# Optimization experiments

Measured on AMD Instinct MI355X. Metric: run time of the kernel, lower is better.

Reference implementation:

```python
import jax, jax.numpy as jnp
import numpy as np

K = 2            # number of attention heads (k in __init__)
NEG = -9.0e15    # mask fill value from the torch code
N, C, CO = 6144, 128, 128


def _ln(x, g, b, eps=1e-5):
    m = x.mean(-1, keepdims=True)
    v = ((x - m) ** 2).mean(-1, keepdims=True)
    return (x - m) / jnp.sqrt(v + eps) * g + b


def setup_inputs() -> dict:
    key = jax.random.key(0)
    ks = jax.random.split(key, 6)
    x = jax.random.normal(ks[0], (N, C), jnp.float32)
    adj = (jax.random.uniform(ks[1], (N, N)) < 0.01).astype(jnp.float32)
    ff0_w = jax.random.normal(ks[2], (K, C, C), jnp.float32) / np.float32(np.sqrt(C))
    ff1_w = jax.random.normal(ks[3], (K, CO, C), jnp.float32) / np.float32(np.sqrt(C))
    attn_w = jax.random.normal(ks[4], (K, 2 * C), jnp.float32) / np.float32(np.sqrt(2 * C))
    return dict(
        x=x, adj=adj, ff0_w=ff0_w, ff1_w=ff1_w, attn_w=attn_w,
        g1=jnp.ones((C,), jnp.float32), b1=jnp.zeros((C,), jnp.float32),
        g2=jnp.ones((C,), jnp.float32), b2=jnp.zeros((C,), jnp.float32),
    )


def reference(x, adj, ff0_w, ff1_w, attn_w, g1, b1, g2, b2):
    n, c = x.shape
    co = ff1_w.shape[1]
    x_norm = _ln(x, g1, b1)
    # torch does adj = adj + eye(n) each iteration; since adj >= 0 the mask
    # (adj > 0) is identical for every iteration: original edges plus self-loops.
    mask = (adj > 0) | jnp.eye(n, dtype=bool)
    h_next = jnp.zeros((n, co), x.dtype)
    for i in range(K):  # small fixed head count, structurally distinct weights
        h = x_norm @ ff0_w[i].T  # [n, c]
        # attn_fc(cat(h_i, h_j)) == a1.h_i + a2.h_j  (exact decomposition of
        # the concat+linear; avoids materializing the [n, n, 2c] tensor)
        s_src = h @ attn_w[i, :c]  # [n], contribution of row node i
        s_dst = h @ attn_w[i, c:]  # [n], contribution of col node j
        e = jax.nn.leaky_relu(s_src[:, None] + s_dst[None, :])  # [n, n]
        e = jnp.where(mask, e, jnp.float32(NEG))
        atten = jax.nn.softmax(e, axis=1)  # dropout p=0.0 -> identity
        att = atten @ h + x  # residual adds pre-norm x
        att = _ln(att, g2, b2)
        h_next = h_next + jax.nn.elu(att @ ff1_w[i].T) / K
    return h_next
```

## Files before the change

### kernel.cpp

```cpp
#include <hip/hip_runtime.h>
#include <math.h>

#define Nn 6144
#define Cc 128
#define NHD 2
#define GMAXDEG 256
#define FF0_BLOCKS 384

__global__ __launch_bounds__(256) void k_front(
    const float* __restrict__ x, const float* __restrict__ g1,
    const float* __restrict__ b1, const float* __restrict__ Bw,
    const float* __restrict__ aw, const float* __restrict__ adj,
    float* __restrict__ h, float* __restrict__ ssrc,
    float* __restrict__ sdst, int* __restrict__ degp,
    int* __restrict__ nbrg) {
  __shared__ __align__(16) float smem[128 * 36 + 64 * 132];
  const int t = threadIdx.x;
  const int bid = blockIdx.x;

  if (bid >= FF0_BLOCKS) {
    int* nbr = (int*)smem;
    __shared__ int cnt;
    const int r = bid - FF0_BLOCKS;
    if (t == 0) cnt = 0;
    __syncthreads();
    const float4* arow = (const float4*)(adj + (size_t)r * Nn);
    for (int i = t; i < Nn / 4; i += 256) {
      float4 v = arow[i];
      int j = i * 4;
      if (v.x > 0.f || j + 0 == r) { int p = atomicAdd(&cnt, 1); if (p < GMAXDEG) nbr[p] = j + 0; }
      if (v.y > 0.f || j + 1 == r) { int p = atomicAdd(&cnt, 1); if (p < GMAXDEG) nbr[p] = j + 1; }
      if (v.z > 0.f || j + 2 == r) { int p = atomicAdd(&cnt, 1); if (p < GMAXDEG) nbr[p] = j + 2; }
      if (v.w > 0.f || j + 3 == r) { int p = atomicAdd(&cnt, 1); if (p < GMAXDEG) nbr[p] = j + 3; }
    }
    __syncthreads();
    const int d = min(cnt, GMAXDEG);
    if (t == 0) degp[r] = d;
    for (int k = t; k < d; k += 256) nbrg[(size_t)r * GMAXDEG + k] = nbr[k];
    return;
  }

  float (*Axn)[36] = (float(*)[36])smem;
  float (*Bs)[132] = (float(*)[132])(smem + 128 * 36);
  const int head = bid & 1;
  const int row0 = (bid >> 1) * 32;
  const float* Bh = Bw + (size_t)head * Cc * Cc;

  {
    const int row = t >> 3, seg = t & 7;
    const int cb = seg * 16;
    const float* xr = x + (size_t)(row0 + row) * Cc + cb;
    float v[16], gg[16], bb[16];
#pragma unroll
    for (int i = 0; i < 16; i += 4) {
      float4 t4 = *(const float4*)(xr + i);
      v[i] = t4.x; v[i + 1] = t4.y; v[i + 2] = t4.z; v[i + 3] = t4.w;
      float4 g4 = *(const float4*)(g1 + cb + i);
      gg[i] = g4.x; gg[i + 1] = g4.y; gg[i + 2] = g4.z; gg[i + 3] = g4.w;
      float4 b4 = *(const float4*)(b1 + cb + i);
      bb[i] = b4.x; bb[i + 1] = b4.y; bb[i + 2] = b4.z; bb[i + 3] = b4.w;
    }
    float s = 0.f;
#pragma unroll
    for (int i = 0; i < 16; i++) s += v[i];
    s += __shfl_xor(s, 1); s += __shfl_xor(s, 2); s += __shfl_xor(s, 4);
    float mean = s * (1.0f / 128.0f);
    float q = 0.f;
#pragma unroll
    for (int i = 0; i < 16; i++) { float d_ = v[i] - mean; q += d_ * d_; }
    q += __shfl_xor(q, 1); q += __shfl_xor(q, 2); q += __shfl_xor(q, 4);
    float rstd = rsqrtf(q * (1.0f / 128.0f) + 1e-5f);
#pragma unroll
    for (int i = 0; i < 16; i++)
      Axn[cb + i][row] = (v[i] - mean) * rstd * gg[i] + bb[i];
  }
  __syncthreads();

  const int tr = t & 7, tc = t >> 3;
  float acc[4][4];
#pragma unroll
  for (int i = 0; i < 4; i++)
#pragma unroll
    for (int j = 0; j < 4; j++) acc[i][j] = 0.f;

  for (int kt = 0; kt < Cc; kt += 64) {
    for (int i = t; i < 2048; i += 256) {
      int cc2 = i >> 4, k4 = i & 15;
      float4 v = *(const float4*)(Bh + (size_t)cc2 * Cc + kt + k4 * 4);
      Bs[k4 * 4 + 0][cc2] = v.x; Bs[k4 * 4 + 1][cc2] = v.y;
      Bs[k4 * 4 + 2][cc2] = v.z; Bs[k4 * 4 + 3][cc2] = v.w;
    }
    __syncthreads();
#pragma unroll
    for (int k = 0; k < 64; k++) {
      float4 a4 = *(const float4*)&Axn[kt + k][tr * 4];
      float4 b4 = *(const float4*)&Bs[k][tc * 4];
      float av[4] = {a4.x, a4.y, a4.z, a4.w};
      float bv[4] = {b4.x, b4.y, b4.z, b4.w};
#pragma unroll
      for (int i = 0; i < 4; i++)
#pragma unroll
        for (int j = 0; j < 4; j++) acc[i][j] = fmaf(av[i], bv[j], acc[i][j]);
    }
    __syncthreads();
  }

  float psrc[4], pdst[4];
  {
    float4 w1 = *(const float4*)(aw + head * 2 * Cc + tc * 4);
    float4 w2 = *(const float4*)(aw + head * 2 * Cc + Cc + tc * 4);
#pragma unroll
    for (int i = 0; i < 4; i++) {
      float* op = h + ((size_t)head * Nn + row0 + tr * 4 + i) * Cc + tc * 4;
      *(float4*)op = make_float4(acc[i][0], acc[i][1], acc[i][2], acc[i][3]);
      psrc[i] = acc[i][0] * w1.x + acc[i][1] * w1.y + acc[i][2] * w1.z + acc[i][3] * w1.w;
      pdst[i] = acc[i][0] * w2.x + acc[i][1] * w2.y + acc[i][2] * w2.z + acc[i][3] * w2.w;
    }
  }
  float* epart = &Bs[0][0];
#pragma unroll
  for (int i = 0; i < 4; i++) {
    epart[((tc * 32) + (tr * 4 + i)) * 2 + 0] = psrc[i];
    epart[((tc * 32) + (tr * 4 + i)) * 2 + 1] = pdst[i];
  }
  __syncthreads();
  if (t < 64) {
    int row = t >> 1, s = t & 1;
    float v = 0.f;
#pragma unroll
    for (int g = 0; g < 32; g++) v += epart[(g * 32 + row) * 2 + s];
    (s ? sdst : ssrc)[head * Nn + row0 + row] = v;
  }
}

__global__ __launch_bounds__(256) void k_attn_wave(
    const int* __restrict__ degp, const int* __restrict__ nbrg,
    const float* __restrict__ x, const float* __restrict__ h,
    const float* __restrict__ ssrc, const float* __restrict__ sdst,
    const float* __restrict__ g2, const float* __restrict__ b2,
    float* __restrict__ att_out) {
  const int t = threadIdx.x;
  const int lane = t & 63;
  const int r = blockIdx.x * 4 + (t >> 6);
  const int deg = min(degp[r], 128);
  int nbr0 = r, nbr1 = r;
  if (lane < deg) nbr0 = nbrg[(size_t)r * GMAXDEG + lane];
  if (64 + lane < deg) nbr1 = nbrg[(size_t)r * GMAXDEG + 64 + lane];
  const float s0 = ssrc[r], s1 = ssrc[Nn + r];
  float e0a = -3.0e38f, e0b = -3.0e38f, e1a = -3.0e38f, e1b = -3.0e38f;
  if (lane < deg) {
    float v0 = s0 + sdst[nbr0], v1 = s1 + sdst[Nn + nbr0];
    e0a = (v0 > 0.f) ? v0 : 0.01f * v0;
    e1a = (v1 > 0.f) ? v1 : 0.01f * v1;
  }
  if (64 + lane < deg) {
    float v0 = s0 + sdst[nbr1], v1 = s1 + sdst[Nn + nbr1];
    e0b = (v0 > 0.f) ? v0 : 0.01f * v0;
    e1b = (v1 > 0.f) ? v1 : 0.01f * v1;
  }
  float m0 = fmaxf(e0a, e0b), m1 = fmaxf(e1a, e1b);
#pragma unroll
  for (int o = 32; o; o >>= 1) {
    m0 = fmaxf(m0, __shfl_xor(m0, o));
    m1 = fmaxf(m1, __shfl_xor(m1, o));
  }
  float w0a = __expf(e0a - m0), w0b = __expf(e0b - m0);
  float w1a = __expf(e1a - m1), w1b = __expf(e1b - m1);
  float l0 = w0a + w0b, l1 = w1a + w1b;
#pragma unroll
  for (int o = 32; o; o >>= 1) { l0 += __shfl_xor(l0, o); l1 += __shfl_xor(l1, o); }
  const float inv0 = 1.0f / l0, inv1 = 1.0f / l1;
  const int c2 = lane * 2;
  const float* h0p = h + c2;
  const float* h1p = h + (size_t)Nn * Cc + c2;
  float a0x = 0.f, a0y = 0.f, a1x = 0.f, a1y = 0.f;
  for (int k = 0; k < deg; ++k) {
    const bool lo = (k < 64);
    const int ksel = k & 63;
    int j = __shfl(lo ? nbr0 : nbr1, ksel);
    float w0 = __shfl(lo ? w0a : w0b, ksel);
    float w1 = __shfl(lo ? w1a : w1b, ksel);
    float2 hv0 = *(const float2*)(h0p + (size_t)j * Cc);
    float2 hv1 = *(const float2*)(h1p + (size_t)j * Cc);
    a0x = fmaf(w0, hv0.x, a0x); a0y = fmaf(w0, hv0.y, a0y);
    a1x = fmaf(w1, hv1.x, a1x); a1y = fmaf(w1, hv1.y, a1y);
  }
  float2 xv = *(const float2*)(x + (size_t)r * Cc + c2);
  a0x = fmaf(a0x, inv0, xv.x); a0y = fmaf(a0y, inv0, xv.y);
  a1x = fmaf(a1x, inv1, xv.x); a1y = fmaf(a1y, inv1, xv.y);
  float t0 = a0x + a0y, t1 = a1x + a1y;
#pragma unroll
  for (int o = 32; o; o >>= 1) { t0 += __shfl_xor(t0, o); t1 += __shfl_xor(t1, o); }
  float mu0 = t0 * (1.0f / 128.0f), mu1 = t1 * (1.0f / 128.0f);
  float d0x = a0x - mu0, d0y = a0y - mu0;
  float d1x = a1x - mu1, d1y = a1y - mu1;
  float q0 = d0x * d0x + d0y * d0y, q1 = d1x * d1x + d1y * d1y;
#pragma unroll
  for (int o = 32; o; o >>= 1) { q0 += __shfl_xor(q0, o); q1 += __shfl_xor(q1, o); }
  float rs0 = rsqrtf(q0 * (1.0f / 128.0f) + 1e-5f);
  float rs1 = rsqrtf(q1 * (1.0f / 128.0f) + 1e-5f);
  float2 gv = *(const float2*)(g2 + c2);
  float2 bv = *(const float2*)(b2 + c2);
  *(float2*)(att_out + ((size_t)r) * Cc + c2) =
      make_float2(d0x * rs0 * gv.x + bv.x, d0y * rs0 * gv.y + bv.y);
  *(float2*)(att_out + ((size_t)Nn + r) * Cc + c2) =
      make_float2(d1x * rs1 * gv.x + bv.x, d1y * rs1 * gv.y + bv.y);
}

__global__ __launch_bounds__(256) void k_ff1_comb(const float* __restrict__ A,
                                                  const float* __restrict__ Bw,
                                                  float* __restrict__ out) {
  __shared__ float As[64][36];
  __shared__ float Bs[64][132];
  const int t = threadIdx.x;
  const int row0 = blockIdx.x * 32;
  const int tr = t & 7, tc = t >> 3;
  float sum[4][4];
#pragma unroll
  for (int i = 0; i < 4; i++)
#pragma unroll
    for (int j = 0; j < 4; j++) sum[i][j] = 0.f;

  for (int head = 0; head < NHD; head++) {
    const float* Ah = A + (size_t)head * Nn * Cc;
    const float* Bh = Bw + (size_t)head * Cc * Cc;
    float acc[4][4];
#pragma unroll
    for (int i = 0; i < 4; i++)
#pragma unroll
      for (int j = 0; j < 4; j++) acc[i][j] = 0.f;

    for (int kt = 0; kt < Cc; kt += 64) {
      __syncthreads();
      for (int i = t; i < 512; i += 256) {
        int rr = i >> 4, k4 = i & 15;
        float4 v = *(const float4*)(Ah + (size_t)(row0 + rr) * Cc + kt + k4 * 4);
        As[k4 * 4 + 0][rr] = v.x; As[k4 * 4 + 1][rr] = v.y;
        As[k4 * 4 + 2][rr] = v.z; As[k4 * 4 + 3][rr] = v.w;
      }
      for (int i = t; i < 2048; i += 256) {
        int cc2 = i >> 4, k4 = i & 15;
        float4 v = *(const float4*)(Bh + (size_t)cc2 * Cc + kt + k4 * 4);
        Bs[k4 * 4 + 0][cc2] = v.x; Bs[k4 * 4 + 1][cc2] = v.y;
        Bs[k4 * 4 + 2][cc2] = v.z; Bs[k4 * 4 + 3][cc2] = v.w;
      }
      __syncthreads();
#pragma unroll
      for (int k = 0; k < 64; k++) {
        float4 a4 = *(const float4*)&As[k][tr * 4];
        float4 b4 = *(const float4*)&Bs[k][tc * 4];
        float av[4] = {a4.x, a4.y, a4.z, a4.w};
        float bv[4] = {b4.x, b4.y, b4.z, b4.w};
#pragma unroll
        for (int i = 0; i < 4; i++)
#pragma unroll
          for (int j = 0; j < 4; j++) acc[i][j] = fmaf(av[i], bv[j], acc[i][j]);
      }
    }
#pragma unroll
    for (int i = 0; i < 4; i++)
#pragma unroll
      for (int j = 0; j < 4; j++) {
        float v = acc[i][j];
        v = (v > 0.f) ? v : (expf(v) - 1.f);
        sum[i][j] = fmaf(v, 0.5f, sum[i][j]);
      }
  }
#pragma unroll
  for (int i = 0; i < 4; i++) {
    float* op = out + (size_t)(row0 + tr * 4 + i) * Cc + tc * 4;
    *(float4*)op = make_float4(sum[i][0], sum[i][1], sum[i][2], sum[i][3]);
  }
}

extern "C" void kernel_launch(void* const* d_in, const int* in_sizes, int n_in,
                              void* d_out, int out_size, void* d_ws, size_t ws_size,
                              hipStream_t stream) {
  const float* x   = (const float*)d_in[0];
  const float* adj = (const float*)d_in[1];
  const float* ff0 = (const float*)d_in[2];
  const float* ff1 = (const float*)d_in[3];
  const float* aw  = (const float*)d_in[4];
  const float* g1  = (const float*)d_in[5];
  const float* b1  = (const float*)d_in[6];
  const float* g2  = (const float*)d_in[7];
  const float* b2  = (const float*)d_in[8];
  float* out = (float*)d_out;

  float* ws   = (float*)d_ws;
  float* h    = ws;
  float* ssrc = h + (size_t)2 * Nn * Cc;
  float* sdst = ssrc + 2 * Nn;
  float* attn = sdst + 2 * Nn;
  int* degp   = (int*)(attn + (size_t)2 * Nn * Cc);
  int* nbrg   = degp + Nn;

  hipLaunchKernelGGL(k_front, dim3(FF0_BLOCKS + Nn), dim3(256), 0, stream,
                     x, g1, b1, ff0, aw, adj, h, ssrc, sdst, degp, nbrg);
  hipLaunchKernelGGL(k_attn_wave, dim3(Nn / 4), dim3(256), 0, stream,
                     degp, nbrg, x, h, ssrc, sdst, g2, b2, attn);
  hipLaunchKernelGGL(k_ff1_comb, dim3(Nn / 32), dim3(256), 0, stream, attn, ff1, out);
}
```

Baseline: 303.0 us.

## Fuse adjacency scan into attention kernel with wave ballot compaction

Moves the per-row adjacency scan out of the front kernel into the attention kernel, where each wave compacts its row's neighbours into LDS using ballot and popcount prefix sums instead of shared atomics. This removes the global neighbour-list write and read round trip and the atomic contention. In exchange, the large adjacency read no longer overlaps with the ff0 GEMM and runs inside the attention kernel with fewer waves per row.

```diff
diff --git a/kernel.cpp b/kernel.cpp
--- a/kernel.cpp
+++ b/kernel.cpp
@@ -4,46 +4,18 @@
 #define Nn 6144
 #define Cc 128
 #define NHD 2
-#define GMAXDEG 256
-#define FF0_BLOCKS 384
-
-__global__ __launch_bounds__(256) void k_front(
+#define WMAXDEG 128
+
+__global__ __launch_bounds__(256) void k_ff0_fused(
     const float* __restrict__ x, const float* __restrict__ g1,
     const float* __restrict__ b1, const float* __restrict__ Bw,
-    const float* __restrict__ aw, const float* __restrict__ adj,
-    float* __restrict__ h, float* __restrict__ ssrc,
-    float* __restrict__ sdst, int* __restrict__ degp,
-    int* __restrict__ nbrg) {
-  __shared__ __align__(16) float smem[128 * 36 + 64 * 132];
+    const float* __restrict__ aw, float* __restrict__ h,
+    float* __restrict__ ssrc, float* __restrict__ sdst) {
+  __shared__ float Axn[128][36];
+  __shared__ float Bs[64][132];
   const int t = threadIdx.x;
-  const int bid = blockIdx.x;
-
-  if (bid >= FF0_BLOCKS) {
-    int* nbr = (int*)smem;
-    __shared__ int cnt;
-    const int r = bid - FF0_BLOCKS;
-    if (t == 0) cnt = 0;
-    __syncthreads();
-    const float4* arow = (const float4*)(adj + (size_t)r * Nn);
-    for (int i = t; i < Nn / 4; i += 256) {
-      float4 v = arow[i];
-      int j = i * 4;
-      if (v.x > 0.f || j + 0 == r) { int p = atomicAdd(&cnt, 1); if (p < GMAXDEG) nbr[p] = j + 0; }
-      if (v.y > 0.f || j + 1 == r) { int p = atomicAdd(&cnt, 1); if (p < GMAXDEG) nbr[p] = j + 1; }
-      if (v.z > 0.f || j + 2 == r) { int p = atomicAdd(&cnt, 1); if (p < GMAXDEG) nbr[p] = j + 2; }
-      if (v.w > 0.f || j + 3 == r) { int p = atomicAdd(&cnt, 1); if (p < GMAXDEG) nbr[p] = j + 3; }
-    }
-    __syncthreads();
-    const int d = min(cnt, GMAXDEG);
-    if (t == 0) degp[r] = d;
-    for (int k = t; k < d; k += 256) nbrg[(size_t)r * GMAXDEG + k] = nbr[k];
-    return;
-  }
-
-  float (*Axn)[36] = (float(*)[36])smem;
-  float (*Bs)[132] = (float(*)[132])(smem + 128 * 36);
-  const int head = bid & 1;
-  const int row0 = (bid >> 1) * 32;
+  const int head = blockIdx.y;
+  const int row0 = blockIdx.x * 32;
   const float* Bh = Bw + (size_t)head * Cc * Cc;
 
   {
@@ -133,19 +105,53 @@
   }
 }
 
-__global__ __launch_bounds__(256) void k_attn_wave(
-    const int* __restrict__ degp, const int* __restrict__ nbrg,
-    const float* __restrict__ x, const float* __restrict__ h,
-    const float* __restrict__ ssrc, const float* __restrict__ sdst,
-    const float* __restrict__ g2, const float* __restrict__ b2,
-    float* __restrict__ att_out) {
+__global__ __launch_bounds__(256) void k_attn_hybrid(
+    const float* __restrict__ adj, const float* __restrict__ x,
+    const float* __restrict__ h, const float* __restrict__ ssrc,
+    const float* __restrict__ sdst, const float* __restrict__ g2,
+    const float* __restrict__ b2, float* __restrict__ att_out) {
+  __shared__ int nbrs[4][WMAXDEG];
   const int t = threadIdx.x;
   const int lane = t & 63;
-  const int r = blockIdx.x * 4 + (t >> 6);
-  const int deg = min(degp[r], 128);
+  const int wid = t >> 6;
+  const int r = blockIdx.x * 4 + wid;
+  int* nbrw = nbrs[wid];
+  int cnt = 0;
+  const float4* arow = (const float4*)(adj + (size_t)r * Nn);
+  const unsigned long long lmask = (lane == 63) ? 0x7fffffffffffffffull
+                                                : ((1ull << lane) - 1ull);
+  for (int i = lane; i < Nn / 4; i += 64) {
+    float4 v = arow[i];
+    int j = i * 4;
+    {
+      bool p = (v.x > 0.f) || (j == r);
+      unsigned long long m = __ballot(p);
+      if (p) { int pos = cnt + (int)__popcll(m & lmask); if (pos < WMAXDEG) nbrw[pos] = j; }
+      cnt += (int)__popcll(m);
+    }
+    {
+      bool p = (v.y > 0.f) || (j + 1 == r);
+      unsigned long long m = __ballot(p);
+      if (p) { int pos = cnt + (int)__popcll(m & lmask); if (pos < WMAXDEG) nbrw[pos] = j + 1; }
+      cnt += (int)__popcll(m);
+    }
+    {
+      bool p = (v.z > 0.f) || (j + 2 == r);
+      unsigned long long m = __ballot(p);
+      if (p) { int pos = cnt + (int)__popcll(m & lmask); if (pos < WMAXDEG) nbrw[pos] = j + 2; }
+      cnt += (int)__popcll(m);
+    }
+    {
+      bool p = (v.w > 0.f) || (j + 3 == r);
+      unsigned long long m = __ballot(p);
+      if (p) { int pos = cnt + (int)__popcll(m & lmask); if (pos < WMAXDEG) nbrw[pos] = j + 3; }
+      cnt += (int)__popcll(m);
+    }
+  }
+  const int deg = min(cnt, WMAXDEG);
   int nbr0 = r, nbr1 = r;
-  if (lane < deg) nbr0 = nbrg[(size_t)r * GMAXDEG + lane];
-  if (64 + lane < deg) nbr1 = nbrg[(size_t)r * GMAXDEG + 64 + lane];
+  if (lane < deg) nbr0 = nbrw[lane];
+  if (64 + lane < deg) nbr1 = nbrw[64 + lane];
   const float s0 = ssrc[r], s1 = ssrc[Nn + r];
   float e0a = -3.0e38f, e0b = -3.0e38f, e1a = -3.0e38f, e1b = -3.0e38f;
   if (lane < deg) {
@@ -292,12 +298,10 @@
   float* ssrc = h + (size_t)2 * Nn * Cc;
   float* sdst = ssrc + 2 * Nn;
   float* attn = sdst + 2 * Nn;
-  int* degp   = (int*)(attn + (size_t)2 * Nn * Cc);
-  int* nbrg   = degp + Nn;
-
-  hipLaunchKernelGGL(k_front, dim3(FF0_BLOCKS + Nn), dim3(256), 0, stream,
-                     x, g1, b1, ff0, aw, adj, h, ssrc, sdst, degp, nbrg);
-  hipLaunchKernelGGL(k_attn_wave, dim3(Nn / 4), dim3(256), 0, stream,
-                     degp, nbrg, x, h, ssrc, sdst, g2, b2, attn);
+
+  hipLaunchKernelGGL(k_ff0_fused, dim3(Nn / 32, NHD), dim3(256), 0, stream,
+                     x, g1, b1, ff0, aw, h, ssrc, sdst);
+  hipLaunchKernelGGL(k_attn_hybrid, dim3(Nn / 4), dim3(256), 0, stream,
+                     adj, x, h, ssrc, sdst, g2, b2, attn);
   hipLaunchKernelGGL(k_ff1_comb, dim3(Nn / 32), dim3(256), 0, stream, attn, ff1, out);
 }
```

Result: no change. 303.5 us (+0.2%).

## Split adjacency scan from ff0 GEMM and shrink GEMM tiles for more blocks

Applied to the files above, without the earlier changes.

Splits the combined front kernel into a separate adjacency-scan kernel and an ff0+layernorm+score kernel. The ff0 GEMM tile goes from 32 to 16 rows with a 2D grid over heads. The ff1 GEMM tile goes to 16 rows by 64 columns, which raises the block count to give more parallelism. The cost is an extra launch, the loss of overlap between the scan and the GEMM, and more redundant loads of the weight matrices across the smaller tiles.

```diff
diff --git a/kernel.cpp b/kernel.cpp
--- a/kernel.cpp
+++ b/kernel.cpp
@@ -5,54 +5,50 @@
 #define Cc 128
 #define NHD 2
 #define GMAXDEG 256
-#define FF0_BLOCKS 384
-
-__global__ __launch_bounds__(256) void k_front(
+
+__global__ __launch_bounds__(256) void k_scan(const float* __restrict__ adj,
+                                              int* __restrict__ degp,
+                                              int* __restrict__ nbrg) {
+  __shared__ int nbr[GMAXDEG];
+  __shared__ int cnt;
+  const int t = threadIdx.x;
+  const int r = blockIdx.x;
+  if (t == 0) cnt = 0;
+  __syncthreads();
+  const float4* arow = (const float4*)(adj + (size_t)r * Nn);
+  for (int i = t; i < Nn / 4; i += 256) {
+    float4 v = arow[i];
+    int j = i * 4;
+    if (v.x > 0.f || j + 0 == r) { int p = atomicAdd(&cnt, 1); if (p < GMAXDEG) nbr[p] = j + 0; }
+    if (v.y > 0.f || j + 1 == r) { int p = atomicAdd(&cnt, 1); if (p < GMAXDEG) nbr[p] = j + 1; }
+    if (v.z > 0.f || j + 2 == r) { int p = atomicAdd(&cnt, 1); if (p < GMAXDEG) nbr[p] = j + 2; }
+    if (v.w > 0.f || j + 3 == r) { int p = atomicAdd(&cnt, 1); if (p < GMAXDEG) nbr[p] = j + 3; }
+  }
+  __syncthreads();
+  const int d = min(cnt, GMAXDEG);
+  if (t == 0) degp[r] = d;
+  for (int k = t; k < d; k += 256) nbrg[(size_t)r * GMAXDEG + k] = nbr[k];
+}
+
+__global__ __launch_bounds__(256) void k_ff0_fused(
     const float* __restrict__ x, const float* __restrict__ g1,
     const float* __restrict__ b1, const float* __restrict__ Bw,
-    const float* __restrict__ aw, const float* __restrict__ adj,
-    float* __restrict__ h, float* __restrict__ ssrc,
-    float* __restrict__ sdst, int* __restrict__ degp,
-    int* __restrict__ nbrg) {
-  __shared__ __align__(16) float smem[128 * 36 + 64 * 132];
-  const int t = threadIdx.x;
-  const int bid = blockIdx.x;
-
-  if (bid >= FF0_BLOCKS) {
-    int* nbr = (int*)smem;
-    __shared__ int cnt;
-    const int r = bid - FF0_BLOCKS;
-    if (t == 0) cnt = 0;
-    __syncthreads();
-    const float4* arow = (const float4*)(adj + (size_t)r * Nn);
-    for (int i = t; i < Nn / 4; i += 256) {
-      float4 v = arow[i];
-      int j = i * 4;
-      if (v.x > 0.f || j + 0 == r) { int p = atomicAdd(&cnt, 1); if (p < GMAXDEG) nbr[p] = j + 0; }
-      if (v.y > 0.f || j + 1 == r) { int p = atomicAdd(&cnt, 1); if (p < GMAXDEG) nbr[p] = j + 1; }
-      if (v.z > 0.f || j + 2 == r) { int p = atomicAdd(&cnt, 1); if (p < GMAXDEG) nbr[p] = j + 2; }
-      if (v.w > 0.f || j + 3 == r) { int p = atomicAdd(&cnt, 1); if (p < GMAXDEG) nbr[p] = j + 3; }
-    }
-    __syncthreads();
-    const int d = min(cnt, GMAXDEG);
-    if (t == 0) degp[r] = d;
-    for (int k = t; k < d; k += 256) nbrg[(size_t)r * GMAXDEG + k] = nbr[k];
-    return;
-  }
-
-  float (*Axn)[36] = (float(*)[36])smem;
-  float (*Bs)[132] = (float(*)[132])(smem + 128 * 36);
-  const int head = bid & 1;
-  const int row0 = (bid >> 1) * 32;
+    const float* __restrict__ aw, float* __restrict__ h,
+    float* __restrict__ ssrc, float* __restrict__ sdst) {
+  __shared__ float Axn[128][18];
+  __shared__ float Bs[64][132];
+  const int t = threadIdx.x;
+  const int head = blockIdx.y;
+  const int row0 = blockIdx.x * 16;
   const float* Bh = Bw + (size_t)head * Cc * Cc;
 
   {
-    const int row = t >> 3, seg = t & 7;
-    const int cb = seg * 16;
+    const int row = t >> 4, seg = t & 15;
+    const int cb = seg * 8;
     const float* xr = x + (size_t)(row0 + row) * Cc + cb;
-    float v[16], gg[16], bb[16];
-#pragma unroll
-    for (int i = 0; i < 16; i += 4) {
+    float v[8], gg[8], bb[8];
+#pragma unroll
+    for (int i = 0; i < 8; i += 4) {
       float4 t4 = *(const float4*)(xr + i);
       v[i] = t4.x; v[i + 1] = t4.y; v[i + 2] = t4.z; v[i + 3] = t4.w;
       float4 g4 = *(const float4*)(g1 + cb + i);
@@ -62,24 +58,26 @@
     }
     float s = 0.f;
 #pragma unroll
-    for (int i = 0; i < 16; i++) s += v[i];
-    s += __shfl_xor(s, 1); s += __shfl_xor(s, 2); s += __shfl_xor(s, 4);
+    for (int i = 0; i < 8; i++) s += v[i];
+    s += __shfl_xor(s, 1); s += __shfl_xor(s, 2);
+    s += __shfl_xor(s, 4); s += __shfl_xor(s, 8);
     float mean = s * (1.0f / 128.0f);
     float q = 0.f;
 #pragma unroll
-    for (int i = 0; i < 16; i++) { float d_ = v[i] - mean; q += d_ * d_; }
-    q += __shfl_xor(q, 1); q += __shfl_xor(q, 2); q += __shfl_xor(q, 4);
+    for (int i = 0; i < 8; i++) { float d_ = v[i] - mean; q += d_ * d_; }
+    q += __shfl_xor(q, 1); q += __shfl_xor(q, 2);
+    q += __shfl_xor(q, 4); q += __shfl_xor(q, 8);
     float rstd = rsqrtf(q * (1.0f / 128.0f) + 1e-5f);
 #pragma unroll
-    for (int i = 0; i < 16; i++)
+    for (int i = 0; i < 8; i++)
       Axn[cb + i][row] = (v[i] - mean) * rstd * gg[i] + bb[i];
   }
   __syncthreads();
 
   const int tr = t & 7, tc = t >> 3;
-  float acc[4][4];
-#pragma unroll
-  for (int i = 0; i < 4; i++)
+  float acc[2][4];
+#pragma unroll
+  for (int i = 0; i < 2; i++)
 #pragma unroll
     for (int j = 0; j < 4; j++) acc[i][j] = 0.f;
 
@@ -93,25 +91,27 @@
     __syncthreads();
 #pragma unroll
     for (int k = 0; k < 64; k++) {
-      float4 a4 = *(const float4*)&Axn[kt + k][tr * 4];
+      float2 a2 = *(const float2*)&Axn[kt + k][tr * 2];
       float4 b4 = *(const float4*)&Bs[k][tc * 4];
-      float av[4] = {a4.x, a4.y, a4.z, a4.w};
-      float bv[4] = {b4.x, b4.y, b4.z, b4.w};
-#pragma unroll
-      for (int i = 0; i < 4; i++)
-#pragma unroll
-        for (int j = 0; j < 4; j++) acc[i][j] = fmaf(av[i], bv[j], acc[i][j]);
+      acc[0][0] = fmaf(a2.x, b4.x, acc[0][0]);
+      acc[0][1] = fmaf(a2.x, b4.y, acc[0][1]);
+      acc[0][2] = fmaf(a2.x, b4.z, acc[0][2]);
+      acc[0][3] = fmaf(a2.x, b4.w, acc[0][3]);
+      acc[1][0] = fmaf(a2.y, b4.x, acc[1][0]);
+      acc[1][1] = fmaf(a2.y, b4.y, acc[1][1]);
+      acc[1][2] = fmaf(a2.y, b4.z, acc[1][2]);
+      acc[1][3] = fmaf(a2.y, b4.w, acc[1][3]);
     }
     __syncthreads();
   }
 
-  float psrc[4], pdst[4];
+  float psrc[2], pdst[2];
   {
     float4 w1 = *(const float4*)(aw + head * 2 * Cc + tc * 4);
     float4 w2 = *(const float4*)(aw + head * 2 * Cc + Cc + tc * 4);
 #pragma unroll
-    for (int i = 0; i < 4; i++) {
-      float* op = h + ((size_t)head * Nn + row0 + tr * 4 + i) * Cc + tc * 4;
+    for (int i = 0; i < 2; i++) {
+      float* op = h + ((size_t)head * Nn + row0 + tr * 2 + i) * Cc + tc * 4;
       *(float4*)op = make_float4(acc[i][0], acc[i][1], acc[i][2], acc[i][3]);
       psrc[i] = acc[i][0] * w1.x + acc[i][1] * w1.y + acc[i][2] * w1.z + acc[i][3] * w1.w;
       pdst[i] = acc[i][0] * w2.x + acc[i][1] * w2.y + acc[i][2] * w2.z + acc[i][3] * w2.w;
@@ -119,16 +119,16 @@
   }
   float* epart = &Bs[0][0];
 #pragma unroll
-  for (int i = 0; i < 4; i++) {
-    epart[((tc * 32) + (tr * 4 + i)) * 2 + 0] = psrc[i];
-    epart[((tc * 32) + (tr * 4 + i)) * 2 + 1] = pdst[i];
-  }
-  __syncthreads();
-  if (t < 64) {
+  for (int i = 0; i < 2; i++) {
+    epart[(tc * 16 + tr * 2 + i) * 2 + 0] = psrc[i];
+    epart[(tc * 16 + tr * 2 + i) * 2 + 1] = pdst[i];
+  }
+  __syncthreads();
+  if (t < 32) {
     int row = t >> 1, s = t & 1;
     float v = 0.f;
 #pragma unroll
-    for (int g = 0; g < 32; g++) v += epart[(g * 32 + row) * 2 + s];
+    for (int g = 0; g < 32; g++) v += epart[(g * 16 + row) * 2 + s];
     (s ? sdst : ssrc)[head * Nn + row0 + row] = v;
   }
 }
@@ -210,66 +210,59 @@
 __global__ __launch_bounds__(256) void k_ff1_comb(const float* __restrict__ A,
                                                   const float* __restrict__ Bw,
                                                   float* __restrict__ out) {
-  __shared__ float As[64][36];
-  __shared__ float Bs[64][132];
-  const int t = threadIdx.x;
-  const int row0 = blockIdx.x * 32;
+  __shared__ float As[128][18];
+  __shared__ float Bs[64][68];
+  const int t = threadIdx.x;
+  const int row0 = blockIdx.x * 16;
+  const int c0 = blockIdx.y * 64;
   const int tr = t & 7, tc = t >> 3;
-  float sum[4][4];
-#pragma unroll
-  for (int i = 0; i < 4; i++)
-#pragma unroll
-    for (int j = 0; j < 4; j++) sum[i][j] = 0.f;
+  float sum[2][2];
+  sum[0][0] = sum[0][1] = sum[1][0] = sum[1][1] = 0.f;
 
   for (int head = 0; head < NHD; head++) {
     const float* Ah = A + (size_t)head * Nn * Cc;
     const float* Bh = Bw + (size_t)head * Cc * Cc;
-    float acc[4][4];
-#pragma unroll
-    for (int i = 0; i < 4; i++)
-#pragma unroll
-      for (int j = 0; j < 4; j++) acc[i][j] = 0.f;
-
+    __syncthreads();
+    for (int i = t; i < 512; i += 256) {
+      int rr = i >> 5, k4 = i & 31;
+      float4 v = *(const float4*)(Ah + (size_t)(row0 + rr) * Cc + k4 * 4);
+      As[k4 * 4 + 0][rr] = v.x; As[k4 * 4 + 1][rr] = v.y;
+      As[k4 * 4 + 2][rr] = v.z; As[k4 * 4 + 3][rr] = v.w;
+    }
+    float acc[2][2];
+    acc[0][0] = acc[0][1] = acc[1][0] = acc[1][1] = 0.f;
     for (int kt = 0; kt < Cc; kt += 64) {
-      __syncthreads();
-      for (int i = t; i < 512; i += 256) {
-        int rr = i >> 4, k4 = i & 15;
-        float4 v = *(const float4*)(Ah + (size_t)(row0 + rr) * Cc + kt + k4 * 4);
-        As[k4 * 4 + 0][rr] = v.x; As[k4 * 4 + 1][rr] = v.y;
-        As[k4 * 4 + 2][rr] = v.z; As[k4 * 4 + 3][rr] = v.w;
-      }
-      for (int i = t; i < 2048; i += 256) {
+      if (kt) __syncthreads();
+      for (int i = t; i < 1024; i += 256) {
         int cc2 = i >> 4, k4 = i & 15;
-        float4 v = *(const float4*)(Bh + (size_t)cc2 * Cc + kt + k4 * 4);
+        float4 v = *(const float4*)(Bh + (size_t)(c0 + cc2) * Cc + kt + k4 * 4);
         Bs[k4 * 4 + 0][cc2] = v.x; Bs[k4 * 4 + 1][cc2] = v.y;
         Bs[k4 * 4 + 2][cc2] = v.z; Bs[k4 * 4 + 3][cc2] = v.w;
       }
       __syncthreads();
 #pragma unroll
       for (int k = 0; k < 64; k++) {
-        float4 a4 = *(const float4*)&As[k][tr * 4];
-        float4 b4 = *(const float4*)&Bs[k][tc * 4];
-        float av[4] = {a4.x, a4.y, a4.z, a4.w};
-        float bv[4] = {b4.x, b4.y, b4.z, b4.w};
-#pragma unroll
-        for (int i = 0; i < 4; i++)
-#pragma unroll
-          for (int j = 0; j < 4; j++) acc[i][j] = fmaf(av[i], bv[j], acc[i][j]);
+        float2 a2 = *(const float2*)&As[kt + k][tr * 2];
+        float2 b2 = *(const float2*)&Bs[k][tc * 2];
+        acc[0][0] = fmaf(a2.x, b2.x, acc[0][0]);
+        acc[0][1] = fmaf(a2.x, b2.y, acc[0][1]);
+        acc[1][0] = fmaf(a2.y, b2.x, acc[1][0]);
+        acc[1][1] = fmaf(a2.y, b2.y, acc[1][1]);
       }
     }
 #pragma unroll
-    for (int i = 0; i < 4; i++)
-#pragma unroll
-      for (int j = 0; j < 4; j++) {
+    for (int i = 0; i < 2; i++)
+#pragma unroll
+      for (int j = 0; j < 2; j++) {
         float v = acc[i][j];
         v = (v > 0.f) ? v : (expf(v) - 1.f);
         sum[i][j] = fmaf(v, 0.5f, sum[i][j]);
       }
   }
 #pragma unroll
-  for (int i = 0; i < 4; i++) {
-    float* op = out + (size_t)(row0 + tr * 4 + i) * Cc + tc * 4;
-    *(float4*)op = make_float4(sum[i][0], sum[i][1], sum[i][2], sum[i][3]);
+  for (int i = 0; i < 2; i++) {
+    float* op = out + (size_t)(row0 + tr * 2 + i) * Cc + c0 + tc * 2;
+    *(float2*)op = make_float2(sum[i][0], sum[i][1]);
   }
 }
 
@@ -295,9 +288,11 @@
   int* degp   = (int*)(attn + (size_t)2 * Nn * Cc);
   int* nbrg   = degp + Nn;
 
-  hipLaunchKernelGGL(k_front, dim3(FF0_BLOCKS + Nn), dim3(256), 0, stream,
-                     x, g1, b1, ff0, aw, adj, h, ssrc, sdst, degp, nbrg);
+  hipLaunchKernelGGL(k_scan, dim3(Nn), dim3(256), 0, stream, adj, degp, nbrg);
+  hipLaunchKernelGGL(k_ff0_fused, dim3(Nn / 16, NHD), dim3(256), 0, stream,
+                     x, g1, b1, ff0, aw, h, ssrc, sdst);
   hipLaunchKernelGGL(k_attn_wave, dim3(Nn / 4), dim3(256), 0, stream,
                      degp, nbrg, x, h, ssrc, sdst, g2, b2, attn);
-  hipLaunchKernelGGL(k_ff1_comb, dim3(Nn / 32), dim3(256), 0, stream, attn, ff1, out);
-}
+  hipLaunchKernelGGL(k_ff1_comb, dim3(Nn / 16, 2), dim3(256), 0, stream,
+                     attn, ff1, out);
+}
```

Result: slower. 384.4 us (+26.9%).
